# Kernel optimization log

Measured on AMD Instinct MI355X. Metric: run time of the kernel, lower is better.

Reference implementation:

```python
import jax, jax.numpy as jnp
import numpy as np

L, N, D, C = 4, 16384, 512, 1000

def setup_inputs() -> dict:
    key = jax.random.key(0)
    k1, k2, k3, k4, k5 = jax.random.split(key, 5)
    feature = jax.random.normal(k1, (L, N, D), dtype=jnp.float32)
    mean = jax.random.normal(k2, (L, C, D), dtype=jnp.float32)
    inverse_cov = jax.random.normal(k3, (L, D, D), dtype=jnp.float32)
    weight = jax.random.uniform(k4, (L,), dtype=jnp.float32)
    top2_index = jax.random.randint(k5, (N,), 0, C, dtype=jnp.int64)
    return {"feature": feature, "mean": mean, "inverse_cov": inverse_cov,
            "weight": weight, "top2_index": top2_index}

def reference(feature, mean, inverse_cov, weight, top2_index):
    # Gather class means per sample: [L, N, D]
    final_mean = mean[:, top2_index, :]
    zero_f = feature - final_mean  # [L, N, D]
    # Diagonal of zero_f @ inv_cov @ zero_f^T without forming the NxN matrix:
    # q[l, n] = sum_{d,e} zero_f[l,n,d] * inv_cov[l,d,e] * zero_f[l,n,e]
    q = jnp.einsum('lnd,lde,lne->ln', zero_f, inverse_cov, zero_f)  # [L, N]
    return jnp.sum(weight * jnp.mean(q, axis=1))
```

## Files before the change

kernel.cpp:

```cpp
#include <hip/hip_runtime.h>
#include <hip/hip_bf16.h>
#include <stdint.h>

#define LDIM 4
#define NDIM 16384
#define DDIM 512
#define CDIM 1000
#define NSTEP 16

#define SYT_ELEMS ((size_t)LDIM * DDIM * DDIM)
#define GH_OFF   (SYT_ELEMS * 2)
#define GH_ELEMS ((size_t)LDIM * CDIM * DDIM)
#define SS_OFF   (GH_OFF + GH_ELEMS * 2)
#define SS_FLOATS ((size_t)LDIM * 1024)
#define WS_NEED  (SS_OFF + SS_FLOATS * 4)

typedef __attribute__((ext_vector_type(8))) _Float16 f16x8;
typedef __attribute__((ext_vector_type(4))) float f32x4;

__device__ __forceinline__ unsigned short f2h(float x) {
  union { _Float16 h; unsigned short u; } c; c.h = (_Float16)x; return c.u;
}
__device__ __forceinline__ float h2f(unsigned short u) {
  union { unsigned short u; _Float16 h; } c; c.u = u; return (float)c.h;
}
__device__ __forceinline__ f16x8 cvt8(float4 a, float4 b) {
  f16x8 p;
  p[0] = (_Float16)a.x; p[1] = (_Float16)a.y; p[2] = (_Float16)a.z; p[3] = (_Float16)a.w;
  p[4] = (_Float16)b.x; p[5] = (_Float16)b.y; p[6] = (_Float16)b.z; p[7] = (_Float16)b.w;
  return p;
}

__device__ __forceinline__ size_t syt_off(int l, int d, int k) {
  return ((size_t)(l * NSTEP + (k >> 5)) * DDIM + d) * 32 +
         ((((k & 31) >> 3) + ((d >> 1) & 3)) & 3) * 8 + (k & 7);
}

#define IDS_OFF 65536
#define SVAL_OFF 65792
#define RED_OFF 66048
#define LDS_MAIN 66080
#define LDS_PREP 65536

extern "C" __global__ void mel_mconv(const float* __restrict__ IC,
                                     unsigned short* __restrict__ SYT) {
  size_t i4 = (size_t)blockIdx.x * 256 + threadIdx.x;
  size_t base = i4 * 4;
  int l = (int)(base >> 18);
  int rem = (int)(base & 262143);
  int d = rem >> 9;
  int e = rem & 511;
  float4 v = *(const float4*)(IC + base);
  const float* icl = IC + ((size_t)l << 18);
  float t0 = icl[(size_t)(e + 0) * DDIM + d];
  float t1 = icl[(size_t)(e + 1) * DDIM + d];
  float t2 = icl[(size_t)(e + 2) * DDIM + d];
  float t3 = icl[(size_t)(e + 3) * DDIM + d];
  *(ushort4*)(SYT + syt_off(l, d, e)) =
      make_ushort4(f2h(0.5f * (v.x + t0)), f2h(0.5f * (v.y + t1)),
                   f2h(0.5f * (v.z + t2)), f2h(0.5f * (v.w + t3)));
}

extern "C" __global__ __launch_bounds__(512, 2)
void mel_prep(const float* __restrict__ MEAN, const unsigned short* __restrict__ SYT,
              unsigned short* __restrict__ GH, float* __restrict__ SS) {
  extern __shared__ __align__(16) char lds[];
  const int t = threadIdx.x, lane = t & 63, w = t >> 6;
  const int l = blockIdx.x & 3, ct = blockIdx.x >> 2;
  const int row0 = ct * 64;
  const int col0 = w * 64, lrow = lane & 15, lkg = lane >> 4;
  const int lke = lkg << 3;

  {
    const int srow = t >> 3;
    const int grow = row0 + srow;
    const float* mr = MEAN + ((size_t)l * CDIM + grow) * DDIM + ((t & 7) << 3);
    const int swb = srow * 1024 + (((t & 7) ^ (srow & 7)) << 4);
    const float4 z4 = {0.f, 0.f, 0.f, 0.f};
    for (int c = 0; c < 8; ++c) {
      float4 x = z4, y = z4;
      if (grow < CDIM) { x = *(const float4*)(mr + c * 64); y = *(const float4*)(mr + c * 64 + 4); }
      *(f16x8*)(lds + swb + c * 128) = cvt8(x, y);
    }
  }
  __syncthreads();

  f32x4 acc[4][4];
#pragma unroll
  for (int i = 0; i < 4; ++i)
#pragma unroll
    for (int j = 0; j < 4; ++j) acc[i][j] = {0.f, 0.f, 0.f, 0.f};

  for (int c = 0; c < 8; ++c) {
#pragma unroll
    for (int ks = 0; ks < 2; ++ks) {
      const int k = c * 64 + ks * 32 + lke;
      f16x8 b0 = *(const f16x8*)(SYT + syt_off(l, col0 + lrow, k));
      f16x8 b1 = *(const f16x8*)(SYT + syt_off(l, col0 + 16 + lrow, k));
      f16x8 b2 = *(const f16x8*)(SYT + syt_off(l, col0 + 32 + lrow, k));
      f16x8 b3 = *(const f16x8*)(SYT + syt_off(l, col0 + 48 + lrow, k));
      const int xo = c * 128 + ((((ks << 2) + lkg) ^ (lrow & 7)) << 4);
      f16x8 a0 = *(const f16x8*)(lds + lrow * 1024 + xo);
      f16x8 a1 = *(const f16x8*)(lds + (16 + lrow) * 1024 + xo);
      f16x8 a2 = *(const f16x8*)(lds + (32 + lrow) * 1024 + xo);
      f16x8 a3 = *(const f16x8*)(lds + (48 + lrow) * 1024 + xo);
#pragma unroll
      for (int nf = 0; nf < 4; ++nf) {
        f16x8 a = nf == 0 ? a0 : nf == 1 ? a1 : nf == 2 ? a2 : a3;
        acc[nf][0] = __builtin_amdgcn_mfma_f32_16x16x32_f16(a, b0, acc[nf][0], 0, 0, 0);
        acc[nf][1] = __builtin_amdgcn_mfma_f32_16x16x32_f16(a, b1, acc[nf][1], 0, 0, 0);
        acc[nf][2] = __builtin_amdgcn_mfma_f32_16x16x32_f16(a, b2, acc[nf][2], 0, 0, 0);
        acc[nf][3] = __builtin_amdgcn_mfma_f32_16x16x32_f16(a, b3, acc[nf][3], 0, 0, 0);
      }
    }
  }

#pragma unroll
  for (int nf = 0; nf < 4; ++nf)
#pragma unroll
    for (int r = 0; r < 4; ++r) {
      const int nloc = nf * 16 + lkg * 4 + r;
      const int grow = row0 + nloc;
      float sp = 0.f;
#pragma unroll
      for (int df = 0; df < 4; ++df) {
        const int dcol = col0 + df * 16 + lrow;
        const float av = acc[nf][df][r];
        const float mh = h2f(*(const unsigned short*)(
            lds + nloc * 1024 + (((dcol >> 3) ^ (nloc & 7)) << 4) + (dcol & 7) * 2));
        sp += mh * av;
        if (grow < CDIM) GH[((size_t)l * CDIM + grow) * DDIM + dcol] = f2h(2.f * av);
      }
      sp += __shfl_xor(sp, 1); sp += __shfl_xor(sp, 2);
      sp += __shfl_xor(sp, 4); sp += __shfl_xor(sp, 8);
      if (lrow == 0 && grow < CDIM) atomicAdd(SS + l * 1024 + grow, sp);
    }
}

extern "C" __global__ __launch_bounds__(512, 4)
void mel_main(const float* __restrict__ F, const float* __restrict__ W,
              const int* __restrict__ IDX, const unsigned short* __restrict__ SYT,
              const unsigned short* __restrict__ GH, const float* __restrict__ SS,
              float* __restrict__ OUT) {
  extern __shared__ __align__(16) char lds[];
  int* ids = (int*)(lds + IDS_OFF);
  float* sval = (float*)(lds + SVAL_OFF);
  float* red = (float*)(lds + RED_OFF);
  const int t = threadIdx.x, lane = t & 63, w = t >> 6;
  const int bid = blockIdx.x, xcd = bid & 7, l = xcd >> 1;
  const int bx = ((bid >> 3) << 1) | (xcd & 1);
  const int n0 = bx * 64;
  const int col0 = w * 64;
  const int lrow = lane & 15, lkg = lane >> 4;

  if (t < 64) {
    const int cc = IDX[n0 + t];
    ids[t] = cc;
    sval[t] = SS[l * 1024 + cc];
  }

  const int a_row = t >> 3, a_el = (t & 7) << 2;
  const float* fA = F + ((size_t)l * NDIM + n0 + a_row) * DDIM + a_el;
  const int a_wb = a_row * 64 + ((((a_el >> 3) + ((a_row >> 1) & 3)) & 3) << 4) +
                   ((a_el & 7) << 1);
  {
    float4 fv[16];
#pragma unroll
    for (int c = 0; c < 16; ++c) fv[c] = *(const float4*)(fA + c * 32);
#pragma unroll
    for (int c = 0; c < 16; ++c) {
      ushort4 h = make_ushort4(f2h(fv[c].x), f2h(fv[c].y), f2h(fv[c].z), f2h(fv[c].w));
      *(ushort4*)(lds + c * 4096 + a_wb) = h;
    }
  }
  __syncthreads();

  f32x4 acc[4][4];
#pragma unroll
  for (int i = 0; i < 4; ++i)
#pragma unroll
    for (int j = 0; j < 4; ++j) acc[i][j] = {0.f, 0.f, 0.f, 0.f};

#pragma unroll 4
  for (int s = 0; s < NSTEP; ++s) {
    f16x8 bf[4], af[4];
#pragma unroll
    for (int df = 0; df < 4; ++df)
      bf[df] = *(const f16x8*)(SYT + syt_off(l, col0 + df * 16 + lrow, s * 32 + lkg * 8));
#pragma unroll
    for (int nf = 0; nf < 4; ++nf) {
      const int row = nf * 16 + lrow;
      af[nf] = *(const f16x8*)(lds + s * 4096 + row * 64 +
                               (((lkg + ((row >> 1) & 3)) & 3) << 4));
    }
#pragma unroll
    for (int nf = 0; nf < 4; ++nf)
#pragma unroll
      for (int df = 0; df < 4; ++df)
        acc[nf][df] = __builtin_amdgcn_mfma_f32_16x16x32_f16(af[nf], bf[df], acc[nf][df], 0, 0, 0);
  }

  const unsigned short* gh_l = GH + (size_t)l * CDIM * DDIM;
  const float* fre = F + ((size_t)l * NDIM + n0) * DDIM;
  float tsum = 0.f;
#pragma unroll
  for (int nf = 0; nf < 4; ++nf)
#pragma unroll
    for (int df = 0; df < 4; ++df) {
      const int col = col0 + df * 16 + lrow;
      f32x4 cfrag = acc[nf][df];
#pragma unroll
      for (int r = 0; r < 4; ++r) {
        const int rowl = nf * 16 + lkg * 4 + r;
        const float fh = fre[(size_t)rowl * DDIM + col];
        const float gh = h2f(gh_l[(size_t)ids[rowl] * DDIM + col]);
        tsum += fh * (cfrag[r] - gh);
        if (w == 0 && df == 0 && lrow == 0) tsum += sval[rowl];
      }
    }
#pragma unroll
  for (int off = 32; off > 0; off >>= 1) tsum += __shfl_down(tsum, off);
  __syncthreads();
  if (lane == 0) red[w] = tsum;
  __syncthreads();
  if (t == 0) {
    float ssum = 0.f;
#pragma unroll
    for (int i = 0; i < 8; ++i) ssum += red[i];
    atomicAdd(OUT, ssum * (W[l] / (float)NDIM));
  }
}

extern "C" __global__ void mel_fallback(const float* __restrict__ F,
                                        const float* __restrict__ MEAN,
                                        const float* __restrict__ IC,
                                        const float* __restrict__ W,
                                        const int* __restrict__ IDX,
                                        float* __restrict__ OUT) {
  __shared__ float v[8][DDIM];
  __shared__ float red[256];
  const int t = threadIdx.x;
  const int l = blockIdx.y;
  const int n0 = blockIdx.x * 8;
  for (int i = t; i < 8 * DDIM; i += 256) {
    int n = i >> 9, e = i & 511;
    int c = IDX[n0 + n];
    v[n][e] = F[((size_t)l * NDIM + n0 + n) * DDIM + e] -
              MEAN[((size_t)l * CDIM + c) * DDIM + e];
  }
  __syncthreads();
  const float* icl = IC + ((size_t)l << 18);
  float part = 0.f;
  for (int rep = 0; rep < 2; ++rep) {
    int d = t + rep * 256;
    float s[8];
#pragma unroll
    for (int j = 0; j < 8; ++j) s[j] = 0.f;
    for (int e = 0; e < DDIM; ++e) {
      float m = icl[(size_t)d * DDIM + e];
#pragma unroll
      for (int j = 0; j < 8; ++j) s[j] += m * v[j][e];
    }
#pragma unroll
    for (int j = 0; j < 8; ++j) part += v[j][d] * s[j];
  }
  red[t] = part;
  __syncthreads();
  for (int o = 128; o > 0; o >>= 1) {
    if (t < o) red[t] += red[t + o];
    __syncthreads();
  }
  if (t == 0) atomicAdd(OUT, red[0] * (W[l] / (float)NDIM));
}

extern "C" void kernel_launch(void* const* d_in, const int* in_sizes, int n_in,
                              void* d_out, int out_size, void* d_ws, size_t ws_size,
                              hipStream_t stream) {
  const float* F = (const float*)d_in[0];
  const float* MEAN = (const float*)d_in[1];
  const float* IC = (const float*)d_in[2];
  const float* W = (const float*)d_in[3];
  const int* IDX = (const int*)d_in[4];
  float* OUT = (float*)d_out;

  hipMemsetAsync(d_out, 0, sizeof(float) * (size_t)out_size, stream);

  if (ws_size >= WS_NEED) {
    unsigned short* SYTp = (unsigned short*)d_ws;
    unsigned short* GHp = (unsigned short*)((char*)d_ws + GH_OFF);
    float* SSp = (float*)((char*)d_ws + SS_OFF);
    hipMemsetAsync(SSp, 0, SS_FLOATS * 4, stream);
    mel_mconv<<<dim3(1024), dim3(256), 0, stream>>>(IC, SYTp);
    (void)hipFuncSetAttribute(reinterpret_cast<const void*>(mel_prep),
                              hipFuncAttributeMaxDynamicSharedMemorySize, LDS_PREP);
    mel_prep<<<dim3(64), dim3(512), LDS_PREP, stream>>>(MEAN, SYTp, GHp, SSp);
    (void)hipFuncSetAttribute(reinterpret_cast<const void*>(mel_main),
                              hipFuncAttributeMaxDynamicSharedMemorySize, LDS_MAIN);
    mel_main<<<dim3(1024), dim3(512), LDS_MAIN, stream>>>(
        F, W, IDX, SYTp, GHp, SSp, OUT);
  } else {
    mel_fallback<<<dim3(NDIM / 8, LDIM), dim3(256), 0, stream>>>(F, MEAN, IC, W, IDX, OUT);
  }
}
```

Measured before the change: 96.64 us.

## Pipeline feature staging into LDS across MFMA k-steps and reuse LDS fp16 in epilogue

The up-front load of the whole 64x512 feature tile into LDS is split into four chunks. Each next chunk's global loads are issued before the MFMA work on the current chunk, then converted to fp16 and stored to LDS afterwards, so global latency overlaps compute. The epilogue now reads the feature values from the fp16 LDS copy instead of re-reading fp32 from global memory. This removes redundant global traffic but lowers the epilogue term to fp16 precision and adds three barriers.

New measurement: 87.82 us. 1.1x faster.

```diff
diff --git a/kernel.cpp b/kernel.cpp
--- a/kernel.cpp
+++ b/kernel.cpp
@@ -163,15 +163,16 @@
   const float* fA = F + ((size_t)l * NDIM + n0 + a_row) * DDIM + a_el;
   const int a_wb = a_row * 64 + ((((a_el >> 3) + ((a_row >> 1) & 3)) & 3) << 4) +
                    ((a_el & 7) << 1);
+
   {
-    float4 fv[16];
-#pragma unroll
-    for (int c = 0; c < 16; ++c) fv[c] = *(const float4*)(fA + c * 32);
-#pragma unroll
-    for (int c = 0; c < 16; ++c) {
-      ushort4 h = make_ushort4(f2h(fv[c].x), f2h(fv[c].y), f2h(fv[c].z), f2h(fv[c].w));
-      *(ushort4*)(lds + c * 4096 + a_wb) = h;
-    }
+    float4 x0 = *(const float4*)(fA);
+    float4 x1 = *(const float4*)(fA + 32);
+    float4 x2 = *(const float4*)(fA + 64);
+    float4 x3 = *(const float4*)(fA + 96);
+    *(ushort4*)(lds + 0 * 4096 + a_wb) = make_ushort4(f2h(x0.x), f2h(x0.y), f2h(x0.z), f2h(x0.w));
+    *(ushort4*)(lds + 1 * 4096 + a_wb) = make_ushort4(f2h(x1.x), f2h(x1.y), f2h(x1.z), f2h(x1.w));
+    *(ushort4*)(lds + 2 * 4096 + a_wb) = make_ushort4(f2h(x2.x), f2h(x2.y), f2h(x2.z), f2h(x2.w));
+    *(ushort4*)(lds + 3 * 4096 + a_wb) = make_ushort4(f2h(x3.x), f2h(x3.y), f2h(x3.z), f2h(x3.w));
   }
   __syncthreads();
 
@@ -181,27 +182,46 @@
 #pragma unroll
     for (int j = 0; j < 4; ++j) acc[i][j] = {0.f, 0.f, 0.f, 0.f};
 
-#pragma unroll 4
-  for (int s = 0; s < NSTEP; ++s) {
-    f16x8 bf[4], af[4];
-#pragma unroll
-    for (int df = 0; df < 4; ++df)
-      bf[df] = *(const f16x8*)(SYT + syt_off(l, col0 + df * 16 + lrow, s * 32 + lkg * 8));
-#pragma unroll
-    for (int nf = 0; nf < 4; ++nf) {
-      const int row = nf * 16 + lrow;
-      af[nf] = *(const f16x8*)(lds + s * 4096 + row * 64 +
-                               (((lkg + ((row >> 1) & 3)) & 3) << 4));
-    }
-#pragma unroll
-    for (int nf = 0; nf < 4; ++nf)
+#pragma unroll
+  for (int q = 0; q < 4; ++q) {
+    float4 n0v, n1v, n2v, n3v;
+    if (q < 3) {
+      const float* fn = fA + (q + 1) * 128;
+      n0v = *(const float4*)(fn);
+      n1v = *(const float4*)(fn + 32);
+      n2v = *(const float4*)(fn + 64);
+      n3v = *(const float4*)(fn + 96);
+    }
+#pragma unroll
+    for (int s4 = 0; s4 < 4; ++s4) {
+      const int s = q * 4 + s4;
+      f16x8 bf[4], af[4];
 #pragma unroll
       for (int df = 0; df < 4; ++df)
-        acc[nf][df] = __builtin_amdgcn_mfma_f32_16x16x32_f16(af[nf], bf[df], acc[nf][df], 0, 0, 0);
+        bf[df] = *(const f16x8*)(SYT + syt_off(l, col0 + df * 16 + lrow, s * 32 + lkg * 8));
+#pragma unroll
+      for (int nf = 0; nf < 4; ++nf) {
+        const int row = nf * 16 + lrow;
+        af[nf] = *(const f16x8*)(lds + s * 4096 + row * 64 +
+                                 (((lkg + ((row >> 1) & 3)) & 3) << 4));
+      }
+#pragma unroll
+      for (int nf = 0; nf < 4; ++nf)
+#pragma unroll
+        for (int df = 0; df < 4; ++df)
+          acc[nf][df] = __builtin_amdgcn_mfma_f32_16x16x32_f16(af[nf], bf[df], acc[nf][df], 0, 0, 0);
+    }
+    if (q < 3) {
+      char* base = lds + (q + 1) * 16384;
+      *(ushort4*)(base + 0 * 4096 + a_wb) = make_ushort4(f2h(n0v.x), f2h(n0v.y), f2h(n0v.z), f2h(n0v.w));
+      *(ushort4*)(base + 1 * 4096 + a_wb) = make_ushort4(f2h(n1v.x), f2h(n1v.y), f2h(n1v.z), f2h(n1v.w));
+      *(ushort4*)(base + 2 * 4096 + a_wb) = make_ushort4(f2h(n2v.x), f2h(n2v.y), f2h(n2v.z), f2h(n2v.w));
+      *(ushort4*)(base + 3 * 4096 + a_wb) = make_ushort4(f2h(n3v.x), f2h(n3v.y), f2h(n3v.z), f2h(n3v.w));
+      __syncthreads();
+    }
   }
 
   const unsigned short* gh_l = GH + (size_t)l * CDIM * DDIM;
-  const float* fre = F + ((size_t)l * NDIM + n0) * DDIM;
   float tsum = 0.f;
 #pragma unroll
   for (int nf = 0; nf < 4; ++nf)
@@ -212,7 +232,9 @@
 #pragma unroll
       for (int r = 0; r < 4; ++r) {
         const int rowl = nf * 16 + lkg * 4 + r;
-        const float fh = fre[(size_t)rowl * DDIM + col];
+        const float fh = h2f(*(const unsigned short*)(
+            lds + (col >> 5) * 4096 + rowl * 64 +
+            (((((col & 31) >> 3) + ((rowl >> 1) & 3)) & 3) << 4) + ((col & 7) << 1)));
         const float gh = h2f(gh_l[(size_t)ids[rowl] * DDIM + col]);
         tsum += fh * (cfrag[r] - gh);
         if (w == 0 && df == 0 && lrow == 0) tsum += sval[rowl];
```

## Retile main kernel to 256x128 tiles with double-buffered K-phase feature staging

Applied to the files above, without the earlier changes.

Each block now computes a 256-row by 128-column output tile (4x2 wave grid) instead of 64 rows by all 512 columns, streaming the feature rows through LDS in 64-wide K phases with a double buffer. Global loads for the next phase are issued before the MFMAs of the current phase and written to the alternate buffer afterward, overlapping load latency with compute. The intent is better reuse of the SYT matrix and lower LDS footprint per phase. The cost is more feature re-reads across column strips, extra barriers per phase, and higher register pressure from the prefetch registers.

Result: slower. 121.1 us (+25.3%).

```diff
diff --git a/kernel.cpp b/kernel.cpp
--- a/kernel.cpp
+++ b/kernel.cpp
@@ -7,6 +7,7 @@
 #define DDIM 512
 #define CDIM 1000
 #define NSTEP 16
+#define NPHASE 8
 
 #define SYT_ELEMS ((size_t)LDIM * DDIM * DDIM)
 #define GH_OFF   (SYT_ELEMS * 2)
@@ -37,9 +38,9 @@
 }
 
 #define IDS_OFF 65536
-#define SVAL_OFF 65792
-#define RED_OFF 66048
-#define LDS_MAIN 66080
+#define SVAL_OFF 66560
+#define RED_OFF 67584
+#define LDS_MAIN 67616
 #define LDS_PREP 65536
 
 extern "C" __global__ void mel_mconv(const float* __restrict__ IC,
@@ -148,29 +149,38 @@
   float* red = (float*)(lds + RED_OFF);
   const int t = threadIdx.x, lane = t & 63, w = t >> 6;
   const int bid = blockIdx.x, xcd = bid & 7, l = xcd >> 1;
-  const int bx = ((bid >> 3) << 1) | (xcd & 1);
-  const int n0 = bx * 64;
-  const int col0 = w * 64;
+  const int idx = bid >> 3;
+  const int panel = (idx >> 2) + ((xcd & 1) << 5);
+  const int strip = idx & 3;
+  const int n0 = panel * 256;
+  const int c0 = strip * 128;
+  const int rowg = w >> 1, colg = w & 1;
   const int lrow = lane & 15, lkg = lane >> 4;
 
-  if (t < 64) {
+  if (t < 256) {
     const int cc = IDX[n0 + t];
     ids[t] = cc;
     sval[t] = SS[l * 1024 + cc];
   }
 
-  const int a_row = t >> 3, a_el = (t & 7) << 2;
-  const float* fA = F + ((size_t)l * NDIM + n0 + a_row) * DDIM + a_el;
-  const int a_wb = a_row * 64 + ((((a_el >> 3) + ((a_row >> 1) & 3)) & 3) << 4) +
-                   ((a_el & 7) << 1);
+  const int a_r0 = t >> 3, a_kq = t & 7;
+  const float* fA = F + ((size_t)l * NDIM + n0 + a_r0) * DDIM + (a_kq << 2);
+
   {
-    float4 fv[16];
-#pragma unroll
-    for (int c = 0; c < 16; ++c) fv[c] = *(const float4*)(fA + c * 32);
-#pragma unroll
-    for (int c = 0; c < 16; ++c) {
-      ushort4 h = make_ushort4(f2h(fv[c].x), f2h(fv[c].y), f2h(fv[c].z), f2h(fv[c].w));
-      *(ushort4*)(lds + c * 4096 + a_wb) = h;
+#pragma unroll
+    for (int sub = 0; sub < 2; ++sub) {
+      float4 x[4];
+#pragma unroll
+      for (int j = 0; j < 4; ++j)
+        x[j] = *(const float4*)(fA + (size_t)j * 64 * DDIM + sub * 32);
+#pragma unroll
+      for (int j = 0; j < 4; ++j) {
+        const int row = a_r0 + j * 64;
+        const int g = (a_kq >> 1) + sub * 4;
+        const int gp = (g + ((row >> 1) & 7)) & 7;
+        *(ushort4*)(lds + row * 128 + gp * 16 + (a_kq & 1) * 8) =
+            make_ushort4(f2h(x[j].x), f2h(x[j].y), f2h(x[j].z), f2h(x[j].w));
+      }
     }
   }
   __syncthreads();
@@ -181,23 +191,49 @@
 #pragma unroll
     for (int j = 0; j < 4; ++j) acc[i][j] = {0.f, 0.f, 0.f, 0.f};
 
-#pragma unroll 4
-  for (int s = 0; s < NSTEP; ++s) {
-    f16x8 bf[4], af[4];
-#pragma unroll
-    for (int df = 0; df < 4; ++df)
-      bf[df] = *(const f16x8*)(SYT + syt_off(l, col0 + df * 16 + lrow, s * 32 + lkg * 8));
-#pragma unroll
-    for (int nf = 0; nf < 4; ++nf) {
-      const int row = nf * 16 + lrow;
-      af[nf] = *(const f16x8*)(lds + s * 4096 + row * 64 +
-                               (((lkg + ((row >> 1) & 3)) & 3) << 4));
-    }
-#pragma unroll
-    for (int nf = 0; nf < 4; ++nf)
+#pragma unroll
+  for (int p = 0; p < NPHASE; ++p) {
+    const char* cur = lds + (p & 1) * 32768;
+    char* nxt = lds + ((p + 1) & 1) * 32768;
+#pragma unroll
+    for (int sub = 0; sub < 2; ++sub) {
+      float4 x[4];
+      if (p < NPHASE - 1) {
+        const int ko = (p + 1) * 64 + sub * 32;
+#pragma unroll
+        for (int j = 0; j < 4; ++j)
+          x[j] = *(const float4*)(fA + (size_t)j * 64 * DDIM + ko);
+      }
+      const int s = p * 2 + sub;
+      f16x8 bf[4], af[4];
 #pragma unroll
       for (int df = 0; df < 4; ++df)
-        acc[nf][df] = __builtin_amdgcn_mfma_f32_16x16x32_f16(af[nf], bf[df], acc[nf][df], 0, 0, 0);
+        bf[df] = *(const f16x8*)(SYT + syt_off(l, c0 + colg * 64 + df * 16 + lrow,
+                                               s * 32 + lkg * 8));
+#pragma unroll
+      for (int nf = 0; nf < 4; ++nf) {
+        const int row = rowg * 64 + nf * 16 + lrow;
+        const int kgl = sub * 4 + lkg;
+        af[nf] = *(const f16x8*)(cur + row * 128 +
+                                 (((kgl + ((row >> 1) & 7)) & 7) << 4));
+      }
+#pragma unroll
+      for (int nf = 0; nf < 4; ++nf)
+#pragma unroll
+        for (int df = 0; df < 4; ++df)
+          acc[nf][df] = __builtin_amdgcn_mfma_f32_16x16x32_f16(af[nf], bf[df], acc[nf][df], 0, 0, 0);
+      if (p < NPHASE - 1) {
+#pragma unroll
+        for (int j = 0; j < 4; ++j) {
+          const int row = a_r0 + j * 64;
+          const int g = (a_kq >> 1) + sub * 4;
+          const int gp = (g + ((row >> 1) & 7)) & 7;
+          *(ushort4*)(nxt + row * 128 + gp * 16 + (a_kq & 1) * 8) =
+              make_ushort4(f2h(x[j].x), f2h(x[j].y), f2h(x[j].z), f2h(x[j].w));
+        }
+      }
+    }
+    if (p < NPHASE - 1) __syncthreads();
   }
 
   const unsigned short* gh_l = GH + (size_t)l * CDIM * DDIM;
@@ -207,15 +243,15 @@
   for (int nf = 0; nf < 4; ++nf)
 #pragma unroll
     for (int df = 0; df < 4; ++df) {
-      const int col = col0 + df * 16 + lrow;
+      const int col = c0 + colg * 64 + df * 16 + lrow;
       f32x4 cfrag = acc[nf][df];
 #pragma unroll
       for (int r = 0; r < 4; ++r) {
-        const int rowl = nf * 16 + lkg * 4 + r;
+        const int rowl = rowg * 64 + nf * 16 + lkg * 4 + r;
         const float fh = fre[(size_t)rowl * DDIM + col];
         const float gh = h2f(gh_l[(size_t)ids[rowl] * DDIM + col]);
         tsum += fh * (cfrag[r] - gh);
-        if (w == 0 && df == 0 && lrow == 0) tsum += sval[rowl];
+        if (strip == 0 && colg == 0 && df == 0 && lrow == 0) tsum += sval[rowl];
       }
     }
 #pragma unroll
```

## Stage inverse-cov strip in LDS and stream features directly into MFMA fragments

Applied to the files above, without the earlier changes.

Restructures mel_main so each block handles 256 rows by a 128-column strip of the symmetric inverse-cov matrix. The fp16 SYT strip (128 KB) is loaded into LDS asynchronously via global_load_lds, and feature rows are read from global into registers and converted to fp16 per step with one-step prefetch, instead of staging features in LDS. The aim is better reuse of the matrix tile across more rows and less per-step global B-fragment traffic. The cost is doubled LDS use and occupancy dropping to 2 blocks per CU, plus fp32 feature loads in the inner loop.

After: 144.1 us. 1.49x slower.

```diff
diff --git a/kernel.cpp b/kernel.cpp
--- a/kernel.cpp
+++ b/kernel.cpp
@@ -30,16 +30,21 @@
   p[4] = (_Float16)b.x; p[5] = (_Float16)b.y; p[6] = (_Float16)b.z; p[7] = (_Float16)b.w;
   return p;
 }
+__device__ __forceinline__ void gload16(const void* g, void* l) {
+  __builtin_amdgcn_global_load_lds(
+      (const __attribute__((address_space(1))) void*)g,
+      (__attribute__((address_space(3))) void*)l, 16, 0, 0);
+}
 
 __device__ __forceinline__ size_t syt_off(int l, int d, int k) {
   return ((size_t)(l * NSTEP + (k >> 5)) * DDIM + d) * 32 +
          ((((k & 31) >> 3) + ((d >> 1) & 3)) & 3) * 8 + (k & 7);
 }
 
-#define IDS_OFF 65536
-#define SVAL_OFF 65792
-#define RED_OFF 66048
-#define LDS_MAIN 66080
+#define IDS_OFF 131072
+#define SVAL_OFF 132096
+#define RED_OFF 133120
+#define LDS_MAIN 133152
 #define LDS_PREP 65536
 
 extern "C" __global__ void mel_mconv(const float* __restrict__ IC,
@@ -137,7 +142,7 @@
     }
 }
 
-extern "C" __global__ __launch_bounds__(512, 4)
+extern "C" __global__ __launch_bounds__(512, 2)
 void mel_main(const float* __restrict__ F, const float* __restrict__ W,
               const int* __restrict__ IDX, const unsigned short* __restrict__ SYT,
               const unsigned short* __restrict__ GH, const float* __restrict__ SS,
@@ -148,74 +153,78 @@
   float* red = (float*)(lds + RED_OFF);
   const int t = threadIdx.x, lane = t & 63, w = t >> 6;
   const int bid = blockIdx.x, xcd = bid & 7, l = xcd >> 1;
-  const int bx = ((bid >> 3) << 1) | (xcd & 1);
-  const int n0 = bx * 64;
-  const int col0 = w * 64;
+  const int blkl = (bid >> 3) + ((xcd & 1) << 7);
+  const int strip = blkl & 3;
+  const int n0 = (blkl >> 2) * 256;
+  const int c0 = strip * 128;
   const int lrow = lane & 15, lkg = lane >> 4;
-
-  if (t < 64) {
+  const int wbase = w * 32;
+
+  const unsigned short* syt_strip =
+      SYT + (size_t)l * NSTEP * DDIM * 32 + (size_t)c0 * 32;
+#pragma unroll
+  for (int s = 0; s < NSTEP; ++s)
+    gload16(syt_strip + (size_t)s * DDIM * 32 + t * 8,
+            lds + s * 8192 + ((t & ~63) << 4));
+  if (t < 256) {
     const int cc = IDX[n0 + t];
     ids[t] = cc;
     sval[t] = SS[l * 1024 + cc];
   }
-
-  const int a_row = t >> 3, a_el = (t & 7) << 2;
-  const float* fA = F + ((size_t)l * NDIM + n0 + a_row) * DDIM + a_el;
-  const int a_wb = a_row * 64 + ((((a_el >> 3) + ((a_row >> 1) & 3)) & 3) << 4) +
-                   ((a_el & 7) << 1);
-  {
-    float4 fv[16];
-#pragma unroll
-    for (int c = 0; c < 16; ++c) fv[c] = *(const float4*)(fA + c * 32);
-#pragma unroll
-    for (int c = 0; c < 16; ++c) {
-      ushort4 h = make_ushort4(f2h(fv[c].x), f2h(fv[c].y), f2h(fv[c].z), f2h(fv[c].w));
-      *(ushort4*)(lds + c * 4096 + a_wb) = h;
-    }
-  }
-  __syncthreads();
-
-  f32x4 acc[4][4];
-#pragma unroll
-  for (int i = 0; i < 4; ++i)
-#pragma unroll
-    for (int j = 0; j < 4; ++j) acc[i][j] = {0.f, 0.f, 0.f, 0.f};
-
-#pragma unroll 4
+  __syncthreads();
+
+  f32x4 acc[2][8];
+#pragma unroll
+  for (int i = 0; i < 2; ++i)
+#pragma unroll
+    for (int j = 0; j < 8; ++j) acc[i][j] = {0.f, 0.f, 0.f, 0.f};
+
+  const float* fr0 = F + ((size_t)l * NDIM + n0 + wbase + lrow) * DDIM;
+  const float* fr1 = fr0 + 16 * DDIM;
+  const int k0 = lkg * 8;
+  float4 p00 = *(const float4*)(fr0 + k0);
+  float4 p01 = *(const float4*)(fr0 + k0 + 4);
+  float4 p10 = *(const float4*)(fr1 + k0);
+  float4 p11 = *(const float4*)(fr1 + k0 + 4);
+#pragma unroll
   for (int s = 0; s < NSTEP; ++s) {
-    f16x8 bf[4], af[4];
-#pragma unroll
-    for (int df = 0; df < 4; ++df)
-      bf[df] = *(const f16x8*)(SYT + syt_off(l, col0 + df * 16 + lrow, s * 32 + lkg * 8));
-#pragma unroll
-    for (int nf = 0; nf < 4; ++nf) {
-      const int row = nf * 16 + lrow;
-      af[nf] = *(const f16x8*)(lds + s * 4096 + row * 64 +
-                               (((lkg + ((row >> 1) & 3)) & 3) << 4));
-    }
-#pragma unroll
-    for (int nf = 0; nf < 4; ++nf)
-#pragma unroll
-      for (int df = 0; df < 4; ++df)
-        acc[nf][df] = __builtin_amdgcn_mfma_f32_16x16x32_f16(af[nf], bf[df], acc[nf][df], 0, 0, 0);
+    float4 c00 = p00, c01 = p01, c10 = p10, c11 = p11;
+    if (s + 1 < NSTEP) {
+      const int k1 = (s + 1) * 32 + k0;
+      p00 = *(const float4*)(fr0 + k1);
+      p01 = *(const float4*)(fr0 + k1 + 4);
+      p10 = *(const float4*)(fr1 + k1);
+      p11 = *(const float4*)(fr1 + k1 + 4);
+    }
+    f16x8 af0 = cvt8(c00, c01);
+    f16x8 af1 = cvt8(c10, c11);
+    const char* bs = lds + s * 8192;
+#pragma unroll
+    for (int df = 0; df < 8; ++df) {
+      const int dl = df * 16 + lrow;
+      f16x8 bf = *(const f16x8*)(bs + dl * 64 +
+                                 (((lkg + ((dl >> 1) & 3)) & 3) << 4));
+      acc[0][df] = __builtin_amdgcn_mfma_f32_16x16x32_f16(af0, bf, acc[0][df], 0, 0, 0);
+      acc[1][df] = __builtin_amdgcn_mfma_f32_16x16x32_f16(af1, bf, acc[1][df], 0, 0, 0);
+    }
   }
 
   const unsigned short* gh_l = GH + (size_t)l * CDIM * DDIM;
   const float* fre = F + ((size_t)l * NDIM + n0) * DDIM;
   float tsum = 0.f;
 #pragma unroll
-  for (int nf = 0; nf < 4; ++nf)
-#pragma unroll
-    for (int df = 0; df < 4; ++df) {
-      const int col = col0 + df * 16 + lrow;
+  for (int nf = 0; nf < 2; ++nf)
+#pragma unroll
+    for (int df = 0; df < 8; ++df) {
+      const int col = c0 + df * 16 + lrow;
       f32x4 cfrag = acc[nf][df];
 #pragma unroll
       for (int r = 0; r < 4; ++r) {
-        const int rowl = nf * 16 + lkg * 4 + r;
+        const int rowl = wbase + nf * 16 + lkg * 4 + r;
         const float fh = fre[(size_t)rowl * DDIM + col];
         const float gh = h2f(gh_l[(size_t)ids[rowl] * DDIM + col]);
         tsum += fh * (cfrag[r] - gh);
-        if (w == 0 && df == 0 && lrow == 0) tsum += sval[rowl];
+        if (strip == 0 && df == 0 && lrow == 0) tsum += sval[rowl];
       }
     }
 #pragma unroll
```
